# Kernel optimization log

Hardware: AMD Instinct MI355X
Metric: run time of the kernel (lower is better)

## Reference

```python
import jax, jax.numpy as jnp
import numpy as np


def setup_inputs() -> dict:
    key = jax.random.key(0)
    n, d = 256, 64
    ks = jax.random.split(key, 8)
    x = jax.random.normal(ks[0], (n, d), jnp.float32)
    v = jax.random.normal(ks[1], (n, d), jnp.float32)
    # torch nn.Linear convention: weight shape (out_features, in_features)
    W1 = jax.random.normal(ks[2], (d, d), jnp.float32) * (1.0 / np.sqrt(d))
    b1 = jax.random.normal(ks[3], (d,), jnp.float32) * 0.1
    # W2 scaled small + b2 ~ scaled identity so g = M + M^T is well-conditioned (invertible)
    W2 = jax.random.normal(ks[4], (d * d, d), jnp.float32) * 0.02
    b2 = (3.0 * jnp.eye(d, dtype=jnp.float32)).reshape(d * d) \
         + jax.random.normal(ks[5], (d * d,), jnp.float32) * 0.01
    W3 = jax.random.normal(ks[6], (d, 2 * d), jnp.float32) * (1.0 / np.sqrt(2 * d))
    return {"t": 0, "x": x, "v": v, "W1": W1, "b1": b1, "W2": W2, "b2": b2, "W3": W3}


def reference(t, x, v, W1, b1, W2, b2, W3):
    # Connection_gnew.forward. t is unused (ODE-time placeholder), matching the original.
    n, d = x.shape
    # g network: linear1 -> tanh -> linear2 -> symmetrize
    h = jnp.tanh(x @ W1.T + b1)                      # (n, d)
    M = (h @ W2.T + b2).reshape(n, d, d)             # (n, d, d)
    g = M + jnp.transpose(M, (0, 2, 1))              # symmetric metric (n, d, d)
    g_inv = jnp.linalg.inv(g)
    # Analytic batch jacobian of g_flat wrt x (replaces autograd.functional.jacobian):
    # d M_flat[a]/d x[l] = sum_m W2[a,m] * (1 - h[m]^2) * W1[m,l]; then symmetrize (i<->j).
    s = 1.0 - h * h                                   # tanh' (n, d)
    J = jnp.einsum('am,nm,ml->nal', W2, s, W1).reshape(n, d, d, d)
    J = J + jnp.transpose(J, (0, 2, 1, 3))            # J[n,i,j,l] = d g_{ij} / d x_l
    # einsum('nkl,nijl,njil,nlij->nkij', g_inv, J, J, -J):
    # elementwise triple product over matching indices, then contract l with g_inv.
    T = J * jnp.transpose(J, (0, 2, 1, 3)) * (-jnp.transpose(J, (0, 2, 3, 1)))  # T[n,i,j,l]
    connection = 0.5 * jnp.einsum('nkl,nijl->nkij', g_inv, T)
    # dv[n,k] = -sum_{ij} v_i v_j connection[n,k,i,j]
    dv = -jnp.einsum('ni,nj,nkij->nk', v, v, connection)
    out = jnp.concatenate([v, dv], axis=-1) @ W3.T    # linear3, no bias
    return out
```

## Files before the change

### kernel.cpp

```cpp
#include <hip/hip_runtime.h>
#include <math.h>
#include <stdint.h>


typedef short short8 __attribute__((ext_vector_type(8)));
typedef float f32x4 __attribute__((ext_vector_type(4)));

__device__ __forceinline__ unsigned short f2bf(float f) {
  unsigned int u = __builtin_bit_cast(unsigned int, f);
  u += 0x7fffu + ((u >> 16) & 1u);
  return (unsigned short)(u >> 16);
}

__device__ __forceinline__ short8 as_short8(uint4 u) {
  union { uint4 a; short8 b; } cv; cv.a = u; return cv.b;
}

__global__ __launch_bounds__(256) void prep_w2s_kernel(const float* __restrict__ W2,
                                                       unsigned short* __restrict__ W2sB) {
  int g = blockIdx.x * 256 + threadIdx.x;
  int i = g >> 9, j = (g >> 3) & 63, m8 = (g & 7) << 3;
  const float* pa = &W2[((((i << 6) + j) << 6) + m8)];
  const float* pb = &W2[((((j << 6) + i) << 6) + m8)];
  float4 a0 = *(const float4*)pa, a1 = *(const float4*)(pa + 4);
  float4 b0 = *(const float4*)pb, b1 = *(const float4*)(pb + 4);
  short8 r;
  r[0] = (short)f2bf(a0.x + b0.x); r[1] = (short)f2bf(a0.y + b0.y);
  r[2] = (short)f2bf(a0.z + b0.z); r[3] = (short)f2bf(a0.w + b0.w);
  r[4] = (short)f2bf(a1.x + b1.x); r[5] = (short)f2bf(a1.y + b1.y);
  r[6] = (short)f2bf(a1.z + b1.z); r[7] = (short)f2bf(a1.w + b1.w);
  *(short8*)&W2sB[(size_t)g << 3] = r;
}

__global__ __launch_bounds__(512) void conn_kernel(
    const float* __restrict__ x, const float* __restrict__ v,
    const float* __restrict__ W1, const float* __restrict__ b1,
    const float* __restrict__ b2, const float* __restrict__ W3,
    const unsigned short* __restrict__ W2sB, float* __restrict__ out) {
  __shared__ __align__(16) unsigned short sKT[80 * 80];
  __shared__ __align__(16) float sg[64 * 68];
  __shared__ float spq[8][64];
  __shared__ __align__(16) float sh[64], sv[64], sx[64], sq[64];
  __shared__ __align__(16) float sz2[2][64];

  const int n = blockIdx.x, t = threadIdx.x;
  const int wv = t >> 6, lane = t & 63, ln15 = lane & 15, quad = lane >> 4;
  const int o8 = t >> 3, s8 = t & 7;

  if (t < 64) sx[t] = x[(n << 6) + t];
  else if (t < 128) sv[t - 64] = v[(n << 6) + (t - 64)];
  for (int e = t; e < 1280; e += 512) sKT[5120 + e] = 0;
  __syncthreads();

  {
    const float* w1r = &W1[(o8 << 6) + (s8 << 3)];
    float4 wa = *(const float4*)w1r, wb = *(const float4*)(w1r + 4);
    float4 xa = *(const float4*)&sx[s8 << 3], xb = *(const float4*)&sx[(s8 << 3) + 4];
    float acc = wa.x * xa.x + wa.y * xa.y + wa.z * xa.z + wa.w * xa.w
              + wb.x * xb.x + wb.y * xb.y + wb.z * xb.z + wb.w * xb.w;
    acc += __shfl_xor(acc, 1);
    acc += __shfl_xor(acc, 2);
    acc += __shfl_xor(acc, 4);
    if (s8 == 0) sh[o8] = tanhf(acc + b1[o8]);
  }
  __syncthreads();

  for (int e = t; e < 4096; e += 512) {
    int m = e & 63, l = e >> 6;
    float hm = sh[m];
    sKT[l * 80 + m] = f2bf((1.f - hm * hm) * W1[(m << 6) + l]);
  }
  if (t < 64) sKT[64 * 80 + t] = f2bf(sh[t]);
  __syncthreads();

  short8 bf[5][2];
  #pragma unroll
  for (int tc = 0; tc < 5; ++tc)
    #pragma unroll
    for (int ks = 0; ks < 2; ++ks)
      bf[tc][ks] = *(const short8*)&sKT[(tc * 16 + ln15) * 80 + ks * 32 + quad * 8];

  f32x4 svj[4];
  #pragma unroll
  for (int tr = 0; tr < 4; ++tr) svj[tr] = *(const f32x4*)&sv[tr * 16 + quad * 4];

  float qacc[4] = {0.f, 0.f, 0.f, 0.f};

  const int foff = (ln15 << 6) + quad * 8;
  const unsigned short* sbase = W2sB + ((size_t)(8 * wv) << 12);

  uint4 af[4][2], afn[4][2];
  #pragma unroll
  for (int tc = 0; tc < 4; ++tc) {
    af[tc][0] = *(const uint4*)(sbase + (tc << 10) + foff);
    af[tc][1] = *(const uint4*)(sbase + (tc << 10) + foff + 32);
  }

  for (int ii = 0; ii < 8; ++ii) {
    const unsigned short* spn = W2sB + ((size_t)(8 * wv + ((ii + 1) & 7)) << 12);
    #pragma unroll
    for (int tc = 0; tc < 4; ++tc) {
      afn[tc][0] = *(const uint4*)(spn + (tc << 10) + foff);
      afn[tc][1] = *(const uint4*)(spn + (tc << 10) + foff + 32);
    }
    const int i = 8 * wv + ii;
    const float vi = sv[i];

    #pragma unroll
    for (int tr = 0; tr < 4; ++tr) {
      short8 a0 = as_short8(af[tr][0]), a1 = as_short8(af[tr][1]);
      f32x4 c1[4], c2[4], ce;
      #pragma unroll
      for (int tc = 0; tc < 4; ++tc) {
        f32x4 z4 = {0.f, 0.f, 0.f, 0.f};
        f32x4 u = __builtin_amdgcn_mfma_f32_16x16x32_bf16(a0, bf[tc][0], z4, 0, 0, 0);
        c1[tc]  = __builtin_amdgcn_mfma_f32_16x16x32_bf16(a1, bf[tc][1], u, 0, 0, 0);
        f32x4 w = __builtin_amdgcn_mfma_f32_16x16x32_bf16(bf[tr][0], as_short8(af[tc][0]), z4, 0, 0, 0);
        c2[tc]  = __builtin_amdgcn_mfma_f32_16x16x32_bf16(bf[tr][1], as_short8(af[tc][1]), w, 0, 0, 0);
      }
      {
        f32x4 z4 = {0.f, 0.f, 0.f, 0.f};
        f32x4 u = __builtin_amdgcn_mfma_f32_16x16x32_bf16(a0, bf[4][0], z4, 0, 0, 0);
        ce      = __builtin_amdgcn_mfma_f32_16x16x32_bf16(a1, bf[4][1], u, 0, 0, 0);
      }
      if (ln15 == 0)
        *(f32x4*)&sg[i * 68 + tr * 16 + quad * 4] = ce;

      #pragma unroll
      for (int tc = 0; tc < 4; ++tc) {
        float s = 0.f;
        #pragma unroll
        for (int r = 0; r < 4; ++r) {
          float a = c1[tc][r];
          s = fmaf(a * a * c2[tc][r], svj[tr][r], s);
        }
        qacc[tc] = fmaf(s, vi, qacc[tc]);
      }
    }
    #pragma unroll
    for (int tc = 0; tc < 4; ++tc) { af[tc][0] = afn[tc][0]; af[tc][1] = afn[tc][1]; }
  }

  #pragma unroll
  for (int tc = 0; tc < 4; ++tc) {
    float s = qacc[tc];
    s += __shfl_xor(s, 16, 64);
    s += __shfl_xor(s, 32, 64);
    if (quad == 0) spq[wv][tc * 16 + ln15] = s;
  }
  __syncthreads();

  for (int e = t; e < 4096; e += 512) {
    int r = e >> 6, c = e & 63;
    sg[r * 68 + c] += b2[(r << 6) + c] + b2[(c << 6) + r];
  }
  __syncthreads();

  if (t < 64) {
    float s = spq[0][t] + spq[1][t] + spq[2][t] + spq[3][t]
            + spq[4][t] + spq[5][t] + spq[6][t] + spq[7][t];
    sq[t] = s;
    sz2[0][t] = s / sg[t * 68 + t];
  }
  __syncthreads();

  {
    const int row = o8;
    const float* grow = &sg[row * 68];
    const float dinv = 1.f / grow[row];
    const float qr = sq[row];
    int pb = 0;
    for (int it = 0; it < 20; ++it) {
      float p = 0.f;
      #pragma unroll
      for (int cc = 0; cc < 8; ++cc) {
        int c = (cc << 3) + s8;
        p += grow[c] * sz2[pb][c];
      }
      p += __shfl_xor(p, 1);
      p += __shfl_xor(p, 2);
      p += __shfl_xor(p, 4);
      if (s8 == 0) sz2[pb ^ 1][row] = sz2[pb][row] + (qr - p) * dinv;
      __syncthreads();
      pb ^= 1;
    }
  }

  {
    const float* w3r = &W3[o8 << 7];
    float4 wva = *(const float4*)&w3r[s8 << 3];
    float4 wvb = *(const float4*)&w3r[(s8 << 3) + 4];
    float4 wda = *(const float4*)&w3r[64 + (s8 << 3)];
    float4 wdb = *(const float4*)&w3r[64 + (s8 << 3) + 4];
    float4 va = *(const float4*)&sv[s8 << 3], vb = *(const float4*)&sv[(s8 << 3) + 4];
    float4 za = *(const float4*)&sz2[0][s8 << 3], zb = *(const float4*)&sz2[0][(s8 << 3) + 4];
    float acc = wva.x * va.x + wva.y * va.y + wva.z * va.z + wva.w * va.w
              + wvb.x * vb.x + wvb.y * vb.y + wvb.z * vb.z + wvb.w * vb.w
              + 0.5f * (wda.x * za.x + wda.y * za.y + wda.z * za.z + wda.w * za.w
                      + wdb.x * zb.x + wdb.y * zb.y + wdb.z * zb.z + wdb.w * zb.w);
    acc += __shfl_xor(acc, 1);
    acc += __shfl_xor(acc, 2);
    acc += __shfl_xor(acc, 4);
    if (s8 == 0) out[(n << 6) + o8] = acc;
  }
}

extern "C" void kernel_launch(void* const* d_in, const int* in_sizes, int n_in,
                              void* d_out, int out_size, void* d_ws, size_t ws_size,
                              hipStream_t stream) {
  (void)in_sizes; (void)n_in; (void)out_size; (void)ws_size;
  const float* x  = (const float*)d_in[1];
  const float* v  = (const float*)d_in[2];
  const float* W1 = (const float*)d_in[3];
  const float* b1 = (const float*)d_in[4];
  const float* W2 = (const float*)d_in[5];
  const float* b2 = (const float*)d_in[6];
  const float* W3 = (const float*)d_in[7];
  unsigned short* W2sB = (unsigned short*)d_ws;

  hipLaunchKernelGGL(prep_w2s_kernel, dim3(128), dim3(256), 0, stream, W2, W2sB);
  hipLaunchKernelGGL(conn_kernel, dim3(256), dim3(512), 0, stream,
                     x, v, W1, b1, b2, W3, W2sB, (float*)d_out);
}
```

Baseline: 105.6 us.

## Double block to 1024 threads, splitting i-rows across 16 waves

Raises the per-sample block from 8 to 16 wavefronts, so each wave handles 4 rows of i instead of 8. The W2 register prefetch/double-buffer is dropped in favour of plain loads with a non-unrolled loop, and the MFMA results are consumed immediately per tc rather than held in arrays. The aim is more latency hiding and lower register pressure so the larger block fits. In exchange, 1024-thread blocks cap VGPRs per thread, and losing the prefetch may expose global load latency. Every barrier now synchronises twice as many waves, including the 20 iterations of the solver loop.

```diff
diff --git a/kernel.cpp b/kernel.cpp
--- a/kernel.cpp
+++ b/kernel.cpp
@@ -32,40 +32,40 @@
   *(short8*)&W2sB[(size_t)g << 3] = r;
 }
 
-__global__ __launch_bounds__(512) void conn_kernel(
+__global__ __launch_bounds__(1024) void conn_kernel(
     const float* __restrict__ x, const float* __restrict__ v,
     const float* __restrict__ W1, const float* __restrict__ b1,
     const float* __restrict__ b2, const float* __restrict__ W3,
     const unsigned short* __restrict__ W2sB, float* __restrict__ out) {
   __shared__ __align__(16) unsigned short sKT[80 * 80];
   __shared__ __align__(16) float sg[64 * 68];
-  __shared__ float spq[8][64];
+  __shared__ float spq[16][64];
   __shared__ __align__(16) float sh[64], sv[64], sx[64], sq[64];
   __shared__ __align__(16) float sz2[2][64];
 
   const int n = blockIdx.x, t = threadIdx.x;
   const int wv = t >> 6, lane = t & 63, ln15 = lane & 15, quad = lane >> 4;
-  const int o8 = t >> 3, s8 = t & 7;
+  const int o16 = t >> 4, s16 = t & 15;
 
   if (t < 64) sx[t] = x[(n << 6) + t];
   else if (t < 128) sv[t - 64] = v[(n << 6) + (t - 64)];
-  for (int e = t; e < 1280; e += 512) sKT[5120 + e] = 0;
+  for (int e = t; e < 1280; e += 1024) sKT[5120 + e] = 0;
   __syncthreads();
 
   {
-    const float* w1r = &W1[(o8 << 6) + (s8 << 3)];
-    float4 wa = *(const float4*)w1r, wb = *(const float4*)(w1r + 4);
-    float4 xa = *(const float4*)&sx[s8 << 3], xb = *(const float4*)&sx[(s8 << 3) + 4];
-    float acc = wa.x * xa.x + wa.y * xa.y + wa.z * xa.z + wa.w * xa.w
-              + wb.x * xb.x + wb.y * xb.y + wb.z * xb.z + wb.w * xb.w;
+    const float* w1r = &W1[(o16 << 6) + (s16 << 2)];
+    float4 wa = *(const float4*)w1r;
+    float4 xa = *(const float4*)&sx[s16 << 2];
+    float acc = wa.x * xa.x + wa.y * xa.y + wa.z * xa.z + wa.w * xa.w;
     acc += __shfl_xor(acc, 1);
     acc += __shfl_xor(acc, 2);
     acc += __shfl_xor(acc, 4);
-    if (s8 == 0) sh[o8] = tanhf(acc + b1[o8]);
-  }
-  __syncthreads();
-
-  for (int e = t; e < 4096; e += 512) {
+    acc += __shfl_xor(acc, 8);
+    if (s16 == 0) sh[o16] = tanhf(acc + b1[o16]);
+  }
+  __syncthreads();
+
+  for (int e = t; e < 4096; e += 1024) {
     int m = e & 63, l = e >> 6;
     float hm = sh[m];
     sKT[l * 80 + m] = f2bf((1.f - hm * hm) * W1[(m << 6) + l]);
@@ -80,65 +80,50 @@
     for (int ks = 0; ks < 2; ++ks)
       bf[tc][ks] = *(const short8*)&sKT[(tc * 16 + ln15) * 80 + ks * 32 + quad * 8];
 
-  f32x4 svj[4];
-  #pragma unroll
-  for (int tr = 0; tr < 4; ++tr) svj[tr] = *(const f32x4*)&sv[tr * 16 + quad * 4];
-
   float qacc[4] = {0.f, 0.f, 0.f, 0.f};
 
   const int foff = (ln15 << 6) + quad * 8;
-  const unsigned short* sbase = W2sB + ((size_t)(8 * wv) << 12);
-
-  uint4 af[4][2], afn[4][2];
-  #pragma unroll
-  for (int tc = 0; tc < 4; ++tc) {
-    af[tc][0] = *(const uint4*)(sbase + (tc << 10) + foff);
-    af[tc][1] = *(const uint4*)(sbase + (tc << 10) + foff + 32);
-  }
-
-  for (int ii = 0; ii < 8; ++ii) {
-    const unsigned short* spn = W2sB + ((size_t)(8 * wv + ((ii + 1) & 7)) << 12);
+  const unsigned short* sbase = W2sB + ((size_t)(4 * wv) << 12);
+
+  #pragma unroll 1
+  for (int ii = 0; ii < 4; ++ii) {
+    const unsigned short* sp = sbase + ((size_t)ii << 12);
+    uint4 af[4][2];
     #pragma unroll
     for (int tc = 0; tc < 4; ++tc) {
-      afn[tc][0] = *(const uint4*)(spn + (tc << 10) + foff);
-      afn[tc][1] = *(const uint4*)(spn + (tc << 10) + foff + 32);
+      af[tc][0] = *(const uint4*)(sp + (tc << 10) + foff);
+      af[tc][1] = *(const uint4*)(sp + (tc << 10) + foff + 32);
     }
-    const int i = 8 * wv + ii;
+    const int i = 4 * wv + ii;
     const float vi = sv[i];
 
     #pragma unroll
     for (int tr = 0; tr < 4; ++tr) {
       short8 a0 = as_short8(af[tr][0]), a1 = as_short8(af[tr][1]);
-      f32x4 c1[4], c2[4], ce;
+      f32x4 svj = *(const f32x4*)&sv[tr * 16 + quad * 4];
+      {
+        f32x4 z4 = {0.f, 0.f, 0.f, 0.f};
+        f32x4 u  = __builtin_amdgcn_mfma_f32_16x16x32_bf16(a0, bf[4][0], z4, 0, 0, 0);
+        f32x4 ce = __builtin_amdgcn_mfma_f32_16x16x32_bf16(a1, bf[4][1], u, 0, 0, 0);
+        if (ln15 == 0)
+          *(f32x4*)&sg[i * 68 + tr * 16 + quad * 4] = ce;
+      }
       #pragma unroll
       for (int tc = 0; tc < 4; ++tc) {
         f32x4 z4 = {0.f, 0.f, 0.f, 0.f};
-        f32x4 u = __builtin_amdgcn_mfma_f32_16x16x32_bf16(a0, bf[tc][0], z4, 0, 0, 0);
-        c1[tc]  = __builtin_amdgcn_mfma_f32_16x16x32_bf16(a1, bf[tc][1], u, 0, 0, 0);
-        f32x4 w = __builtin_amdgcn_mfma_f32_16x16x32_bf16(bf[tr][0], as_short8(af[tc][0]), z4, 0, 0, 0);
-        c2[tc]  = __builtin_amdgcn_mfma_f32_16x16x32_bf16(bf[tr][1], as_short8(af[tc][1]), w, 0, 0, 0);
-      }
-      {
-        f32x4 z4 = {0.f, 0.f, 0.f, 0.f};
-        f32x4 u = __builtin_amdgcn_mfma_f32_16x16x32_bf16(a0, bf[4][0], z4, 0, 0, 0);
-        ce      = __builtin_amdgcn_mfma_f32_16x16x32_bf16(a1, bf[4][1], u, 0, 0, 0);
-      }
-      if (ln15 == 0)
-        *(f32x4*)&sg[i * 68 + tr * 16 + quad * 4] = ce;
-
-      #pragma unroll
-      for (int tc = 0; tc < 4; ++tc) {
+        f32x4 u  = __builtin_amdgcn_mfma_f32_16x16x32_bf16(a0, bf[tc][0], z4, 0, 0, 0);
+        f32x4 c1 = __builtin_amdgcn_mfma_f32_16x16x32_bf16(a1, bf[tc][1], u, 0, 0, 0);
+        f32x4 w  = __builtin_amdgcn_mfma_f32_16x16x32_bf16(bf[tr][0], as_short8(af[tc][0]), z4, 0, 0, 0);
+        f32x4 c2 = __builtin_amdgcn_mfma_f32_16x16x32_bf16(bf[tr][1], as_short8(af[tc][1]), w, 0, 0, 0);
         float s = 0.f;
         #pragma unroll
         for (int r = 0; r < 4; ++r) {
-          float a = c1[tc][r];
-          s = fmaf(a * a * c2[tc][r], svj[tr][r], s);
+          float a = c1[r];
+          s = fmaf(a * a * c2[r], svj[r], s);
         }
         qacc[tc] = fmaf(s, vi, qacc[tc]);
       }
     }
-    #pragma unroll
-    for (int tc = 0; tc < 4; ++tc) { af[tc][0] = afn[tc][0]; af[tc][1] = afn[tc][1]; }
   }
 
   #pragma unroll
@@ -150,22 +135,23 @@
   }
   __syncthreads();
 
-  for (int e = t; e < 4096; e += 512) {
+  for (int e = t; e < 4096; e += 1024) {
     int r = e >> 6, c = e & 63;
     sg[r * 68 + c] += b2[(r << 6) + c] + b2[(c << 6) + r];
   }
   __syncthreads();
 
   if (t < 64) {
-    float s = spq[0][t] + spq[1][t] + spq[2][t] + spq[3][t]
-            + spq[4][t] + spq[5][t] + spq[6][t] + spq[7][t];
+    float s = 0.f;
+    #pragma unroll
+    for (int w = 0; w < 16; ++w) s += spq[w][t];
     sq[t] = s;
     sz2[0][t] = s / sg[t * 68 + t];
   }
   __syncthreads();
 
   {
-    const int row = o8;
+    const int row = o16;
     const float* grow = &sg[row * 68];
     const float dinv = 1.f / grow[row];
     const float qr = sq[row];
@@ -173,35 +159,33 @@
     for (int it = 0; it < 20; ++it) {
       float p = 0.f;
       #pragma unroll
-      for (int cc = 0; cc < 8; ++cc) {
-        int c = (cc << 3) + s8;
+      for (int cc = 0; cc < 4; ++cc) {
+        int c = (cc << 4) + s16;
         p += grow[c] * sz2[pb][c];
       }
       p += __shfl_xor(p, 1);
       p += __shfl_xor(p, 2);
       p += __shfl_xor(p, 4);
-      if (s8 == 0) sz2[pb ^ 1][row] = sz2[pb][row] + (qr - p) * dinv;
+      p += __shfl_xor(p, 8);
+      if (s16 == 0) sz2[pb ^ 1][row] = sz2[pb][row] + (qr - p) * dinv;
       __syncthreads();
       pb ^= 1;
     }
   }
 
   {
-    const float* w3r = &W3[o8 << 7];
-    float4 wva = *(const float4*)&w3r[s8 << 3];
-    float4 wvb = *(const float4*)&w3r[(s8 << 3) + 4];
-    float4 wda = *(const float4*)&w3r[64 + (s8 << 3)];
-    float4 wdb = *(const float4*)&w3r[64 + (s8 << 3) + 4];
-    float4 va = *(const float4*)&sv[s8 << 3], vb = *(const float4*)&sv[(s8 << 3) + 4];
-    float4 za = *(const float4*)&sz2[0][s8 << 3], zb = *(const float4*)&sz2[0][(s8 << 3) + 4];
+    const float* w3r = &W3[o16 << 7];
+    float4 wva = *(const float4*)&w3r[s16 << 2];
+    float4 wda = *(const float4*)&w3r[64 + (s16 << 2)];
+    float4 va = *(const float4*)&sv[s16 << 2];
+    float4 za = *(const float4*)&sz2[0][s16 << 2];
     float acc = wva.x * va.x + wva.y * va.y + wva.z * va.z + wva.w * va.w
-              + wvb.x * vb.x + wvb.y * vb.y + wvb.z * vb.z + wvb.w * vb.w
-              + 0.5f * (wda.x * za.x + wda.y * za.y + wda.z * za.z + wda.w * za.w
-                      + wdb.x * zb.x + wdb.y * zb.y + wdb.z * zb.z + wdb.w * zb.w);
+              + 0.5f * (wda.x * za.x + wda.y * za.y + wda.z * za.z + wda.w * za.w);
     acc += __shfl_xor(acc, 1);
     acc += __shfl_xor(acc, 2);
     acc += __shfl_xor(acc, 4);
-    if (s8 == 0) out[(n << 6) + o8] = acc;
+    acc += __shfl_xor(acc, 8);
+    if (s16 == 0) out[(n << 6) + o16] = acc;
   }
 }
 
@@ -219,6 +203,6 @@
   unsigned short* W2sB = (unsigned short*)d_ws;
 
   hipLaunchKernelGGL(prep_w2s_kernel, dim3(128), dim3(256), 0, stream, W2, W2sB);
-  hipLaunchKernelGGL(conn_kernel, dim3(256), dim3(512), 0, stream,
+  hipLaunchKernelGGL(conn_kernel, dim3(256), dim3(1024), 0, stream,
                      x, v, W1, b1, b2, W3, W2sB, (float*)d_out);
 }
```

Measured after the change: 209.0 us. 98.0% more time.

## Split connection kernel into MFMA stage over half-blocks and separate solve stage

Applied to the files above, without the earlier changes.

The single per-sample kernel is split in two. The first kernel launches 512 blocks of 256 threads, each handling half of the i-rows for one sample, and writes the g matrix and partial q vectors to workspace in global memory. The second kernel adds the bias, runs the Jacobi solve and applies the output projection with 256 threads per sample. The aim is to double the number of blocks for better CU occupancy and to shorten the serial solve tail, at the cost of an extra launch, a global round trip of g (4 MB), and recomputing h and the Jacobian operand in both halves.

```diff
diff --git a/kernel.cpp b/kernel.cpp
--- a/kernel.cpp
+++ b/kernel.cpp
@@ -32,40 +32,33 @@
   *(short8*)&W2sB[(size_t)g << 3] = r;
 }
 
-__global__ __launch_bounds__(512) void conn_kernel(
+__global__ __launch_bounds__(256) void connA_kernel(
     const float* __restrict__ x, const float* __restrict__ v,
     const float* __restrict__ W1, const float* __restrict__ b1,
-    const float* __restrict__ b2, const float* __restrict__ W3,
-    const unsigned short* __restrict__ W2sB, float* __restrict__ out) {
+    const unsigned short* __restrict__ W2sB,
+    float* __restrict__ gws, float* __restrict__ qws) {
   __shared__ __align__(16) unsigned short sKT[80 * 80];
-  __shared__ __align__(16) float sg[64 * 68];
-  __shared__ float spq[8][64];
-  __shared__ __align__(16) float sh[64], sv[64], sx[64], sq[64];
-  __shared__ __align__(16) float sz2[2][64];
-
-  const int n = blockIdx.x, t = threadIdx.x;
+  __shared__ float spq[4][64];
+  __shared__ __align__(16) float sh[64], sv[64], sx[64];
+
+  const int bid = blockIdx.x;
+  const int n = bid & 255, half = bid >> 8;
+  const int t = threadIdx.x;
   const int wv = t >> 6, lane = t & 63, ln15 = lane & 15, quad = lane >> 4;
-  const int o8 = t >> 3, s8 = t & 7;
-
-  if (t < 64) sx[t] = x[(n << 6) + t];
-  else if (t < 128) sv[t - 64] = v[(n << 6) + (t - 64)];
-  for (int e = t; e < 1280; e += 512) sKT[5120 + e] = 0;
-  __syncthreads();
-
-  {
-    const float* w1r = &W1[(o8 << 6) + (s8 << 3)];
-    float4 wa = *(const float4*)w1r, wb = *(const float4*)(w1r + 4);
-    float4 xa = *(const float4*)&sx[s8 << 3], xb = *(const float4*)&sx[(s8 << 3) + 4];
-    float acc = wa.x * xa.x + wa.y * xa.y + wa.z * xa.z + wa.w * xa.w
-              + wb.x * xb.x + wb.y * xb.y + wb.z * xb.z + wb.w * xb.w;
-    acc += __shfl_xor(acc, 1);
-    acc += __shfl_xor(acc, 2);
-    acc += __shfl_xor(acc, 4);
-    if (s8 == 0) sh[o8] = tanhf(acc + b1[o8]);
-  }
-  __syncthreads();
-
-  for (int e = t; e < 4096; e += 512) {
+
+  if (t < 64) { sx[t] = x[(n << 6) + t]; sv[t] = v[(n << 6) + t]; }
+  for (int e = t; e < 1280; e += 256) sKT[5120 + e] = 0;
+  __syncthreads();
+
+  if (t < 64) {
+    float acc = b1[t];
+    #pragma unroll 8
+    for (int l = 0; l < 64; ++l) acc += sx[l] * W1[(t << 6) + l];
+    sh[t] = tanhf(acc);
+  }
+  __syncthreads();
+
+  for (int e = t; e < 4096; e += 256) {
     int m = e & 63, l = e >> 6;
     float hm = sh[m];
     sKT[l * 80 + m] = f2bf((1.f - hm * hm) * W1[(m << 6) + l]);
@@ -87,7 +80,8 @@
   float qacc[4] = {0.f, 0.f, 0.f, 0.f};
 
   const int foff = (ln15 << 6) + quad * 8;
-  const unsigned short* sbase = W2sB + ((size_t)(8 * wv) << 12);
+  const int ibase = 32 * half + 8 * wv;
+  const unsigned short* sbase = W2sB + ((size_t)ibase << 12);
 
   uint4 af[4][2], afn[4][2];
   #pragma unroll
@@ -97,13 +91,13 @@
   }
 
   for (int ii = 0; ii < 8; ++ii) {
-    const unsigned short* spn = W2sB + ((size_t)(8 * wv + ((ii + 1) & 7)) << 12);
+    const unsigned short* spn = W2sB + ((size_t)(ibase + ((ii + 1) & 7)) << 12);
     #pragma unroll
     for (int tc = 0; tc < 4; ++tc) {
       afn[tc][0] = *(const uint4*)(spn + (tc << 10) + foff);
       afn[tc][1] = *(const uint4*)(spn + (tc << 10) + foff + 32);
     }
-    const int i = 8 * wv + ii;
+    const int i = ibase + ii;
     const float vi = sv[i];
 
     #pragma unroll
@@ -124,7 +118,7 @@
         ce      = __builtin_amdgcn_mfma_f32_16x16x32_bf16(a1, bf[4][1], u, 0, 0, 0);
       }
       if (ln15 == 0)
-        *(f32x4*)&sg[i * 68 + tr * 16 + quad * 4] = ce;
+        *(f32x4*)&gws[((size_t)n << 12) + (i << 6) + tr * 16 + quad * 4] = ce;
 
       #pragma unroll
       for (int tc = 0; tc < 4; ++tc) {
@@ -150,22 +144,34 @@
   }
   __syncthreads();
 
-  for (int e = t; e < 4096; e += 512) {
+  if (t < 64) qws[(bid << 6) + t] = spq[0][t] + spq[1][t] + spq[2][t] + spq[3][t];
+}
+
+__global__ __launch_bounds__(256) void connB_kernel(
+    const float* __restrict__ v, const float* __restrict__ b2,
+    const float* __restrict__ W3, const float* __restrict__ gws,
+    const float* __restrict__ qws, float* __restrict__ out) {
+  __shared__ __align__(16) float sg[64 * 68];
+  __shared__ __align__(16) float sv[64], sq[64];
+  __shared__ __align__(16) float sz2[2][64];
+
+  const int n = blockIdx.x, t = threadIdx.x;
+  const int row = t >> 2, s4 = t & 3;
+
+  if (t < 64) {
+    sv[t] = v[(n << 6) + t];
+    sq[t] = qws[(n << 6) + t] + qws[(256 * 64) + (n << 6) + t];
+  }
+  for (int e = t; e < 4096; e += 256) {
     int r = e >> 6, c = e & 63;
-    sg[r * 68 + c] += b2[(r << 6) + c] + b2[(c << 6) + r];
-  }
-  __syncthreads();
-
-  if (t < 64) {
-    float s = spq[0][t] + spq[1][t] + spq[2][t] + spq[3][t]
-            + spq[4][t] + spq[5][t] + spq[6][t] + spq[7][t];
-    sq[t] = s;
-    sz2[0][t] = s / sg[t * 68 + t];
-  }
+    sg[r * 68 + c] = gws[((size_t)n << 12) + e] + b2[(r << 6) + c] + b2[(c << 6) + r];
+  }
+  __syncthreads();
+
+  if (t < 64) sz2[0][t] = sq[t] / sg[t * 68 + t];
   __syncthreads();
 
   {
-    const int row = o8;
     const float* grow = &sg[row * 68];
     const float dinv = 1.f / grow[row];
     const float qr = sq[row];
@@ -173,35 +179,34 @@
     for (int it = 0; it < 20; ++it) {
       float p = 0.f;
       #pragma unroll
-      for (int cc = 0; cc < 8; ++cc) {
-        int c = (cc << 3) + s8;
+      for (int cc = 0; cc < 16; ++cc) {
+        int c = (cc << 2) + s4;
         p += grow[c] * sz2[pb][c];
       }
       p += __shfl_xor(p, 1);
       p += __shfl_xor(p, 2);
-      p += __shfl_xor(p, 4);
-      if (s8 == 0) sz2[pb ^ 1][row] = sz2[pb][row] + (qr - p) * dinv;
+      if (s4 == 0) sz2[pb ^ 1][row] = sz2[pb][row] + (qr - p) * dinv;
       __syncthreads();
       pb ^= 1;
     }
   }
 
   {
-    const float* w3r = &W3[o8 << 7];
-    float4 wva = *(const float4*)&w3r[s8 << 3];
-    float4 wvb = *(const float4*)&w3r[(s8 << 3) + 4];
-    float4 wda = *(const float4*)&w3r[64 + (s8 << 3)];
-    float4 wdb = *(const float4*)&w3r[64 + (s8 << 3) + 4];
-    float4 va = *(const float4*)&sv[s8 << 3], vb = *(const float4*)&sv[(s8 << 3) + 4];
-    float4 za = *(const float4*)&sz2[0][s8 << 3], zb = *(const float4*)&sz2[0][(s8 << 3) + 4];
-    float acc = wva.x * va.x + wva.y * va.y + wva.z * va.z + wva.w * va.w
-              + wvb.x * vb.x + wvb.y * vb.y + wvb.z * vb.z + wvb.w * vb.w
-              + 0.5f * (wda.x * za.x + wda.y * za.y + wda.z * za.z + wda.w * za.w
-                      + wdb.x * zb.x + wdb.y * zb.y + wdb.z * zb.z + wdb.w * zb.w);
+    const float* w3r = &W3[row << 7];
+    const int c0 = s4 << 4;
+    float acc = 0.f;
+    #pragma unroll
+    for (int k = 0; k < 4; ++k) {
+      float4 w4 = *(const float4*)&w3r[c0 + (k << 2)];
+      float4 v4 = *(const float4*)&sv[c0 + (k << 2)];
+      float4 d4 = *(const float4*)&w3r[64 + c0 + (k << 2)];
+      float4 z4 = *(const float4*)&sz2[0][c0 + (k << 2)];
+      acc += w4.x * v4.x + w4.y * v4.y + w4.z * v4.z + w4.w * v4.w
+           + 0.5f * (d4.x * z4.x + d4.y * z4.y + d4.z * z4.z + d4.w * z4.w);
+    }
     acc += __shfl_xor(acc, 1);
     acc += __shfl_xor(acc, 2);
-    acc += __shfl_xor(acc, 4);
-    if (s8 == 0) out[(n << 6) + o8] = acc;
+    if (s4 == 0) out[(n << 6) + row] = acc;
   }
 }
 
@@ -217,8 +222,12 @@
   const float* b2 = (const float*)d_in[6];
   const float* W3 = (const float*)d_in[7];
   unsigned short* W2sB = (unsigned short*)d_ws;
+  float* gws = (float*)((char*)d_ws + (512 << 10));
+  float* qws = gws + 256 * 4096;
 
   hipLaunchKernelGGL(prep_w2s_kernel, dim3(128), dim3(256), 0, stream, W2, W2sB);
-  hipLaunchKernelGGL(conn_kernel, dim3(256), dim3(512), 0, stream,
-                     x, v, W1, b1, b2, W3, W2sB, (float*)d_out);
-}
+  hipLaunchKernelGGL(connA_kernel, dim3(512), dim3(256), 0, stream,
+                     x, v, W1, b1, W2sB, gws, qws);
+  hipLaunchKernelGGL(connB_kernel, dim3(256), dim3(256), 0, stream,
+                     v, b2, W3, gws, qws, (float*)d_out);
+}
```

After: 110.8 us. 1.05x slower.
